# Performance work log

Hardware: AMD Instinct MI355X
Metric: run time of the kernel (lower is better)

The kernel has to match this reference:

```python
import jax, jax.numpy as jnp
import numpy as np
import math

B, S, D, H = 2, 4096, 128, 8

def setup_inputs() -> dict:
    key = jax.random.key(0)
    k1, k2, k3, k4 = jax.random.split(key, 4)
    x = jax.random.normal(k1, (B, S, D), dtype=jnp.float32)
    W_q = jax.random.normal(k2, (H, D, D), dtype=jnp.float32) * 0.02
    W_k = jax.random.normal(k3, (H, D, D), dtype=jnp.float32) * 0.02
    # nn.Linear weight: [out_features, in_features] = [D, D*H]
    W_o = jax.random.normal(k4, (D, D * H), dtype=jnp.float32) * (0.02 / math.sqrt(2 * 12))
    return {"x": x, "W_q": W_q, "W_k": W_k, "W_o": W_o}

def reference(x, W_q, W_k, W_o):
    b, s, d = x.shape
    h = W_q.shape[0]
    # Per-head projections of the same (repeated) input x.
    Q = jnp.einsum('bsd,hde->bhse', x, W_q)          # [B,H,S,D]
    K = jnp.einsum('bsd,hde->bhse', x, W_k)          # [B,H,S,D]
    scores = jnp.einsum('bhse,bhte->bhst', Q, K) / math.sqrt(d)  # [B,H,S,S]
    scores = jnp.clip(scores, -10.0, 10.0)
    causal = jnp.tril(jnp.ones((s, s), dtype=bool))  # [S,S]
    scores = jnp.where(causal[None, None], scores, -jnp.inf)
    attn = jax.nn.softmax(scores, axis=-1)           # dropout p=0 -> identity
    y = jnp.einsum('bhst,btd->bhsd', attn, x)        # V == x per head
    y = jnp.transpose(y, (0, 2, 1, 3)).reshape(b, s, h * d)  # [B,S,H*D]
    out = y @ W_o.T                                  # [B,S,D]
    return out
```

## Files before the change

kernel.cpp:

```cpp
#include <hip/hip_runtime.h>
#include <hip/hip_bf16.h>

typedef unsigned short u16;
typedef unsigned int u32;
typedef __attribute__((ext_vector_type(8))) short bf16x8;
typedef __attribute__((ext_vector_type(4))) float f32x4;
typedef __attribute__((ext_vector_type(16))) float f32x16;
typedef __attribute__((ext_vector_type(2))) unsigned int u32x2;
typedef __attribute__((ext_vector_type(4))) unsigned int u32x4;

#define S_LEN 4096
#define DHEAD 128
#define NHEAD 8
#define NBATCH 2

__device__ __forceinline__ u16 f2b(float f) {
  __hip_bfloat16 h = __float2bfloat16(f);
  return *(u16*)&h;
}

__device__ __forceinline__ f32x4 mfma16(bf16x8 a, bf16x8 b, f32x4 c) {
  return __builtin_amdgcn_mfma_f32_16x16x32_bf16(a, b, c, 0, 0, 0);
}
__device__ __forceinline__ f32x16 mfma32(bf16x8 a, bf16x8 b, f32x16 c) {
  return __builtin_amdgcn_mfma_f32_32x32x16_bf16(a, b, c, 0, 0, 0);
}

__device__ __forceinline__ f32x4 zero4() { f32x4 z = {0.f, 0.f, 0.f, 0.f}; return z; }

__device__ __forceinline__ u32 cvtpk(float lo, float hi) {
  u32 r;
  asm("v_cvt_pk_bf16_f32 %0, %1, %2" : "=v"(r) : "v"(lo), "v"(hi));
  return r;
}
__device__ __forceinline__ u32x2 pswap(u32 a, u32 b) {
  return __builtin_amdgcn_permlane32_swap(a, b, false, false);
}

__device__ __forceinline__ void gll16(const u16* g, u16* l) {
  __builtin_amdgcn_global_load_lds(
      (const __attribute__((address_space(1))) u32*)g,
      (__attribute__((address_space(3))) u32*)l, 16, 0, 0);
}

__global__ void k_conv_x(const float* __restrict__ x, u16* __restrict__ xb,
                         u16* __restrict__ VbF) {
  int idx = blockIdx.x * blockDim.x + threadIdx.x;
  float v = x[idx];
  u16 bv = f2b(v);
  xb[idx] = bv;
  int d = idx & 127;
  int bs = idx >> 7;
  int b = bs >> 12;
  int s = bs & 4095;
  int t64 = s >> 6, kh = (s >> 5) & 1, m2 = (s >> 4) & 1;
  int h5v = (s >> 3) & 1, j = s & 7;
  int db = d >> 5;
  int l = (d & 31) + 32 * h5v;
  int g = kh * 8 + m2 * 4 + db;
  VbF[(((size_t)b * 64 + t64) * 16 + g) * 512 + l * 8 + j] = bv;
}

__global__ void k_conv_w(const float* __restrict__ Wq, const float* __restrict__ Wk,
                         const float* __restrict__ Wo, u16* __restrict__ Wqt,
                         u16* __restrict__ Wkt, u16* __restrict__ WoB) {
  int idx = blockIdx.x * blockDim.x + threadIdx.x;
  int h = idx >> 14;
  int d = (idx >> 7) & 127;
  int e = idx & 127;
  int t = (h << 14) + (e << 7) + d;
  Wqt[t] = f2b(Wq[idx]);
  Wkt[t] = f2b(Wk[idx]);
  WoB[idx] = f2b(Wo[idx]);
}

__global__ __launch_bounds__(256) void k_proj(const u16* __restrict__ xb,
                                              const u16* __restrict__ Wqt,
                                              const u16* __restrict__ Wkt,
                                              u16* __restrict__ Qb, u16* __restrict__ KbF) {
  int wid = threadIdx.x >> 6;
  int lane = threadIdx.x & 63;
  int qt = blockIdx.x * 4 + wid;
  int h = blockIdx.y, z = blockIdx.z;
  int b = z >> 1, w = z & 1;
  int bh = b * NHEAD + h;
  int row16 = lane & 15, kgrp = lane >> 4;
  int sb = qt * 32;
  const u16* xp = xb + ((size_t)b * S_LEN + sb) * DHEAD;
  bf16x8 a[2][4];
#pragma unroll
  for (int r = 0; r < 2; ++r)
#pragma unroll
    for (int kc = 0; kc < 4; ++kc)
      a[r][kc] = *(const bf16x8*)(xp + (r * 16 + row16) * DHEAD + kc * 32 + kgrp * 8);

  const u16* Wt = (w == 0 ? Wqt : Wkt) + (size_t)h * DHEAD * DHEAD;
  f32x4 acc[2][8];
#pragma unroll
  for (int r = 0; r < 2; ++r)
#pragma unroll
    for (int nc = 0; nc < 8; ++nc) acc[r][nc] = zero4();
#pragma unroll
  for (int kc = 0; kc < 4; ++kc)
#pragma unroll
    for (int nc = 0; nc < 8; ++nc) {
      bf16x8 bw = *(const bf16x8*)(Wt + (nc * 16 + row16) * DHEAD + kc * 32 + kgrp * 8);
      acc[0][nc] = mfma16(a[0][kc], bw, acc[0][nc]);
      acc[1][nc] = mfma16(a[1][kc], bw, acc[1][nc]);
    }
  if (w == 0) {
    u16* Out = Qb + ((size_t)bh * S_LEN + sb) * DHEAD;
#pragma unroll
    for (int r = 0; r < 2; ++r)
#pragma unroll
      for (int nc = 0; nc < 8; ++nc)
#pragma unroll
        for (int i = 0; i < 4; ++i)
          Out[(size_t)(r * 16 + kgrp * 4 + i) * DHEAD + nc * 16 + row16] =
              f2b(acc[r][nc][i]);
  } else {
#pragma unroll
    for (int r = 0; r < 2; ++r)
#pragma unroll
      for (int nc = 0; nc < 8; ++nc)
#pragma unroll
        for (int i = 0; i < 4; ++i) {
          int key = sb + r * 16 + kgrp * 4 + i;
          int e = nc * 16 + row16;
          int t64 = key >> 6, kh = (key >> 5) & 1;
          int m = e >> 4;
          int l = (key & 31) + 32 * ((e >> 3) & 1);
          int j = e & 7;
          int f = kh * 8 + m;
          KbF[(((size_t)bh * 64 + t64) * 16 + f) * 512 + l * 8 + j] = f2b(acc[r][nc][i]);
        }
  }
}

__global__ __launch_bounds__(512) void k_attn(const u16* __restrict__ Qb,
                                              const u16* __restrict__ KbF,
                                              const u16* __restrict__ VbF,
                                              u16* __restrict__ Yb) {
  int p = blockIdx.x;
  int xcd = p & 7;
  int j2 = p >> 3;
  int bh = xcd + (j2 >= 16 ? 8 : 0);
  int qpj = j2 & 15;
  int b = bh >> 3, h = bh & 7;

  int tid = threadIdx.x;
  int wid = tid >> 6;
  int lane = tid & 63;
  int qr = wid >> 1;
  int kh = wid & 1;
  int l31 = lane & 31, h5 = lane >> 5;

  __shared__ __align__(16) u16 Klds[2][8192];
  __shared__ __align__(16) u16 Vlds[2][8192];
  __shared__ float rsbuf[2][4][32];

  const u16* Kbase = KbF + (size_t)bh * 64 * 16 * 512;
  const u16* Vbase = VbF + (size_t)b * 64 * 16 * 512;

  auto issue = [&](int k0, int buf) {
    int t64 = k0 >> 6;
    const u16* Ks = Kbase + (size_t)t64 * 16 * 512;
    const u16* Vs = Vbase + (size_t)t64 * 16 * 512;
#pragma unroll
    for (int fi = 0; fi < 2; ++fi) {
      int f = wid * 2 + fi;
      gll16(Ks + f * 512 + lane * 8, &Klds[buf][f * 512]);
    }
#pragma unroll
    for (int gi = 0; gi < 2; ++gi) {
      int g = wid * 2 + gi;
      gll16(Vs + g * 512 + lane * 8, &Vlds[buf][g * 512]);
    }
  };

  const float c2 = 0.12754274816295166f;
  const float clip2 = 14.426950408889634f;

  auto runSeg = [&](int qblk) {
    int qb0 = qblk * 128;
    int qw = qb0 + qr * 32;
    int qrow = qw + l31;
    const u16* Qp = Qb + ((size_t)bh * S_LEN + qw) * DHEAD;

    bf16x8 bq[8];
#pragma unroll
    for (int m = 0; m < 8; ++m)
      bq[m] = *(const bf16x8*)(Qp + (size_t)l31 * DHEAD + m * 16 + h5 * 8);

    f32x16 y0 = {0.f}, y1 = {0.f}, y2 = {0.f}, y3 = {0.f};
#pragma unroll
    for (int i = 0; i < 16; ++i) { y0[i] = 0.f; y1[i] = 0.f; y2[i] = 0.f; y3[i] = 0.f; }
    float rs = 0.f;

    auto tilecomp = [&](int buf, int k0) {
      f32x16 sc;
#pragma unroll
      for (int i = 0; i < 16; ++i) sc[i] = 0.f;
#pragma unroll
      for (int m = 0; m < 8; ++m) {
        bf16x8 kf = *(const bf16x8*)&Klds[buf][((kh * 8 + m) * 512) + lane * 8];
        sc = mfma32(kf, bq[m], sc);
      }
      float pf[16];
      int kb = k0 + kh * 32 + h5 * 4;
#pragma unroll
      for (int reg = 0; reg < 16; ++reg) {
        int key = kb + (reg & 3) + 8 * (reg >> 2);
        float v = sc[reg] * c2;
        v = fminf(fmaxf(v, -clip2), clip2);
        float pc = __builtin_amdgcn_exp2f(v);
        pc = (key > qrow) ? 0.0f : pc;
        rs += pc;
        pf[reg] = pc;
      }
      u32 cv0 = cvtpk(pf[0], pf[1]), cv1 = cvtpk(pf[2], pf[3]);
      u32 cv2 = cvtpk(pf[4], pf[5]), cv3 = cvtpk(pf[6], pf[7]);
      u32 cv4 = cvtpk(pf[8], pf[9]), cv5 = cvtpk(pf[10], pf[11]);
      u32 cv6 = cvtpk(pf[12], pf[13]), cv7 = cvtpk(pf[14], pf[15]);
      u32x2 s0 = pswap(cv0, cv2);
      u32x2 s1 = pswap(cv1, cv3);
      u32x2 s2 = pswap(cv4, cv6);
      u32x2 s3 = pswap(cv5, cv7);
      u32x4 pa0u = {s0.x, s1.x, s0.y, s1.y};
      u32x4 pa1u = {s2.x, s3.x, s2.y, s3.y};
      bf16x8 pa0 = __builtin_bit_cast(bf16x8, pa0u);
      bf16x8 pa1 = __builtin_bit_cast(bf16x8, pa1u);
      {
        bf16x8 vf = *(const bf16x8*)&Vlds[buf][((kh * 8 + 0) * 512) + lane * 8];
        y0 = mfma32(pa0, vf, y0);
        vf = *(const bf16x8*)&Vlds[buf][((kh * 8 + 4) * 512) + lane * 8];
        y0 = mfma32(pa1, vf, y0);
        vf = *(const bf16x8*)&Vlds[buf][((kh * 8 + 1) * 512) + lane * 8];
        y1 = mfma32(pa0, vf, y1);
        vf = *(const bf16x8*)&Vlds[buf][((kh * 8 + 5) * 512) + lane * 8];
        y1 = mfma32(pa1, vf, y1);
        vf = *(const bf16x8*)&Vlds[buf][((kh * 8 + 2) * 512) + lane * 8];
        y2 = mfma32(pa0, vf, y2);
        vf = *(const bf16x8*)&Vlds[buf][((kh * 8 + 6) * 512) + lane * 8];
        y2 = mfma32(pa1, vf, y2);
        vf = *(const bf16x8*)&Vlds[buf][((kh * 8 + 3) * 512) + lane * 8];
        y3 = mfma32(pa0, vf, y3);
        vf = *(const bf16x8*)&Vlds[buf][((kh * 8 + 7) * 512) + lane * 8];
        y3 = mfma32(pa1, vf, y3);
      }
    };

    int NT = 2 * qblk + 2;
    issue(0, 0);
    __syncthreads();
    for (int t = 0; t < NT; ++t) {
      int k0 = t * 64;
      int cur = t & 1;
      if (t + 1 < NT) issue(k0 + 64, cur ^ 1);
      tilecomp(cur, k0);
      __syncthreads();
    }

    rs += __shfl_xor(rs, 32, 64);

    float* scr = (qr < 2) ? ((float*)&Klds[0][0] + qr * 4096)
                          : ((float*)&Vlds[0][0] + (qr - 2) * 4096);
    if (kh == 1) {
#pragma unroll
      for (int db = 0; db < 4; ++db) {
        const f32x16& yv = (db == 0) ? y0 : (db == 1) ? y1 : (db == 2) ? y2 : y3;
#pragma unroll
        for (int r4 = 0; r4 < 4; ++r4) {
          f32x4 ch = {yv[r4 * 4 + 0], yv[r4 * 4 + 1], yv[r4 * 4 + 2], yv[r4 * 4 + 3]};
          *(f32x4*)&scr[((db * 4 + r4) * 64 + lane) * 4] = ch;
        }
      }
      if (lane < 32) rsbuf[1][qr][lane] = rs;
    }
    __syncthreads();
    if (kh == 0) {
      rs += rsbuf[1][qr][l31];
      float inv = 1.0f / rs;
      if (lane < 32) rsbuf[0][qr][lane] = inv;
#pragma unroll
      for (int db = 0; db < 4; ++db) {
        f32x16& yv = (db == 0) ? y0 : (db == 1) ? y1 : (db == 2) ? y2 : y3;
#pragma unroll
        for (int r4 = 0; r4 < 4; ++r4) {
          f32x4 ch = *(const f32x4*)&scr[((db * 4 + r4) * 64 + lane) * 4];
#pragma unroll
          for (int k = 0; k < 4; ++k) yv[r4 * 4 + k] += ch[k];
        }
      }
      u16* Yp = Yb + ((size_t)b * S_LEN + qw) * (NHEAD * DHEAD) + h * DHEAD;
#pragma unroll
      for (int db = 0; db < 4; ++db) {
        const f32x16& yv = (db == 0) ? y0 : (db == 1) ? y1 : (db == 2) ? y2 : y3;
#pragma unroll
        for (int reg = 0; reg < 16; ++reg) {
          int qp2 = (reg & 3) + 8 * (reg >> 2) + 4 * h5;
          float rv = rsbuf[0][qr][qp2];
          Yp[(size_t)qp2 * (NHEAD * DHEAD) + db * 32 + l31] = f2b(yv[reg] * rv);
        }
      }
    }
    __syncthreads();
  };

  runSeg(31 - qpj);
  runSeg(qpj);
}

__global__ __launch_bounds__(256) void k_oproj(const u16* __restrict__ Yb,
                                               const u16* __restrict__ WoB,
                                               float* __restrict__ out) {
  int wid = threadIdx.x >> 6;
  int lane = threadIdx.x & 63;
  int mb = (blockIdx.x * 4 + wid) * 32 + blockIdx.y * 16;
  int nb = blockIdx.z * 64;
  int row16 = lane & 15, kgrp = lane >> 4;
  f32x4 acc[4];
#pragma unroll
  for (int nc = 0; nc < 4; ++nc) acc[nc] = zero4();
#pragma unroll 4
  for (int kc = 0; kc < 32; ++kc) {
    bf16x8 a0 = *(const bf16x8*)(Yb + (size_t)(mb + row16) * 1024 + kc * 32 + kgrp * 8);
#pragma unroll
    for (int nc = 0; nc < 4; ++nc) {
      bf16x8 bw =
          *(const bf16x8*)(WoB + (size_t)(nb + nc * 16 + row16) * 1024 + kc * 32 + kgrp * 8);
      acc[nc] = mfma16(a0, bw, acc[nc]);
    }
  }
#pragma unroll
  for (int nc = 0; nc < 4; ++nc)
#pragma unroll
    for (int i = 0; i < 4; ++i)
      out[(size_t)(mb + kgrp * 4 + i) * DHEAD + nb + nc * 16 + row16] = acc[nc][i];
}

extern "C" void kernel_launch(void* const* d_in, const int* in_sizes, int n_in,
                              void* d_out, int out_size, void* d_ws, size_t ws_size,
                              hipStream_t stream) {
  const float* x = (const float*)d_in[0];
  const float* Wq = (const float*)d_in[1];
  const float* Wk = (const float*)d_in[2];
  const float* Wo = (const float*)d_in[3];
  float* out = (float*)d_out;

  char* ws = (char*)d_ws;
  size_t off = 0;
  auto alloc = [&](size_t bytes) -> void* {
    void* p = ws + off;
    off += (bytes + 255) & ~(size_t)255;
    return p;
  };
  const size_t nx = (size_t)NBATCH * S_LEN * DHEAD;
  const size_t nqk = (size_t)NBATCH * NHEAD * S_LEN * DHEAD;
  u16* xb = (u16*)alloc(nx * 2);
  u16* VbF = (u16*)alloc(nx * 2);
  u16* Wqt = (u16*)alloc((size_t)NHEAD * DHEAD * DHEAD * 2);
  u16* Wkt = (u16*)alloc((size_t)NHEAD * DHEAD * DHEAD * 2);
  u16* WoB = (u16*)alloc((size_t)DHEAD * NHEAD * DHEAD * 2);
  u16* Qb = (u16*)alloc(nqk * 2);
  u16* KbF = (u16*)alloc(nqk * 2);
  u16* Yb = (u16*)alloc(nqk * 2);
  (void)ws_size;

  k_conv_x<<<dim3(nx / 256), dim3(256), 0, stream>>>(x, xb, VbF);
  k_conv_w<<<dim3(131072 / 256), dim3(256), 0, stream>>>(Wq, Wk, Wo, Wqt, Wkt, WoB);
  k_proj<<<dim3(S_LEN / 32 / 4, NHEAD, 2 * NBATCH), dim3(256), 0, stream>>>(xb, Wqt, Wkt, Qb, KbF);
  k_attn<<<dim3(256), dim3(512), 0, stream>>>(Qb, KbF, VbF, Yb);
  k_oproj<<<dim3((NBATCH * S_LEN) / 32 / 4, 2, 2), dim3(256), 0, stream>>>(Yb, WoB, out);
}
```

Before: 164.9 us.

## Load V fragments directly to registers, prefetch next tile, skip masking on full tiles

V tiles are no longer staged through LDS. Each wave loads its V fragments from global memory straight into registers, double-buffered one tile ahead, while K stays in LDS. The loop is unrolled by two so buffer indices are static, mask computation is skipped for tiles fully below the diagonal, clamping uses fmed3, and setprio brackets the MFMA bursts. The cross-wave reduction now uses a separate float scratch buffer in two phases. This frees LDS and cuts LDS traffic, at the cost of more registers and uncoalesced-per-wave global V reads.

Result: faster. 158.4 us (-4.0%).

```diff
diff --git a/kernel.cpp b/kernel.cpp
--- a/kernel.cpp
+++ b/kernel.cpp
@@ -156,26 +156,24 @@
   int l31 = lane & 31, h5 = lane >> 5;
 
   __shared__ __align__(16) u16 Klds[2][8192];
-  __shared__ __align__(16) u16 Vlds[2][8192];
+  __shared__ __align__(16) float Scr[8192];
   __shared__ float rsbuf[2][4][32];
 
   const u16* Kbase = KbF + (size_t)bh * 64 * 16 * 512;
   const u16* Vbase = VbF + (size_t)b * 64 * 16 * 512;
 
   auto issue = [&](int k0, int buf) {
-    int t64 = k0 >> 6;
-    const u16* Ks = Kbase + (size_t)t64 * 16 * 512;
-    const u16* Vs = Vbase + (size_t)t64 * 16 * 512;
+    const u16* Ks = Kbase + (size_t)(k0 >> 6) * 16 * 512;
 #pragma unroll
     for (int fi = 0; fi < 2; ++fi) {
       int f = wid * 2 + fi;
       gll16(Ks + f * 512 + lane * 8, &Klds[buf][f * 512]);
     }
-#pragma unroll
-    for (int gi = 0; gi < 2; ++gi) {
-      int g = wid * 2 + gi;
-      gll16(Vs + g * 512 + lane * 8, &Vlds[buf][g * 512]);
-    }
+  };
+  auto vload = [&](bf16x8 (&dst)[8], int k0) {
+    const u16* Vs = Vbase + ((size_t)(k0 >> 6) * 16 + kh * 8) * 512 + lane * 8;
+#pragma unroll
+    for (int g = 0; g < 8; ++g) dst[g] = *(const bf16x8*)(Vs + g * 512);
   };
 
   const float c2 = 0.12754274816295166f;
@@ -192,31 +190,47 @@
     for (int m = 0; m < 8; ++m)
       bq[m] = *(const bf16x8*)(Qp + (size_t)l31 * DHEAD + m * 16 + h5 * 8);
 
-    f32x16 y0 = {0.f}, y1 = {0.f}, y2 = {0.f}, y3 = {0.f};
+    f32x16 y0, y1, y2, y3;
 #pragma unroll
     for (int i = 0; i < 16; ++i) { y0[i] = 0.f; y1[i] = 0.f; y2[i] = 0.f; y3[i] = 0.f; }
     float rs = 0.f;
 
-    auto tilecomp = [&](int buf, int k0) {
+    bf16x8 vA[8], vB[8];
+
+    auto tilecomp = [&](int buf, int k0, bf16x8 (&vc)[8], bf16x8 (&vn)[8], int kn0) {
       f32x16 sc;
 #pragma unroll
       for (int i = 0; i < 16; ++i) sc[i] = 0.f;
+      __builtin_amdgcn_s_setprio(1);
 #pragma unroll
       for (int m = 0; m < 8; ++m) {
         bf16x8 kf = *(const bf16x8*)&Klds[buf][((kh * 8 + m) * 512) + lane * 8];
         sc = mfma32(kf, bq[m], sc);
       }
+      __builtin_amdgcn_s_setprio(0);
+      vload(vn, kn0);
+
       float pf[16];
       int kb = k0 + kh * 32 + h5 * 4;
-#pragma unroll
-      for (int reg = 0; reg < 16; ++reg) {
-        int key = kb + (reg & 3) + 8 * (reg >> 2);
-        float v = sc[reg] * c2;
-        v = fminf(fmaxf(v, -clip2), clip2);
-        float pc = __builtin_amdgcn_exp2f(v);
-        pc = (key > qrow) ? 0.0f : pc;
-        rs += pc;
-        pf[reg] = pc;
+      bool nomask = (k0 + kh * 32 + 31) <= qw;
+      if (nomask) {
+#pragma unroll
+        for (int reg = 0; reg < 16; ++reg) {
+          float v = __builtin_amdgcn_fmed3f(sc[reg] * c2, -clip2, clip2);
+          float pc = __builtin_amdgcn_exp2f(v);
+          rs += pc;
+          pf[reg] = pc;
+        }
+      } else {
+#pragma unroll
+        for (int reg = 0; reg < 16; ++reg) {
+          int key = kb + (reg & 3) + 8 * (reg >> 2);
+          float v = __builtin_amdgcn_fmed3f(sc[reg] * c2, -clip2, clip2);
+          float pc = __builtin_amdgcn_exp2f(v);
+          pc = (key > qrow) ? 0.0f : pc;
+          rs += pc;
+          pf[reg] = pc;
+        }
       }
       u32 cv0 = cvtpk(pf[0], pf[1]), cv1 = cvtpk(pf[2], pf[3]);
       u32 cv2 = cvtpk(pf[4], pf[5]), cv3 = cvtpk(pf[6], pf[7]);
@@ -230,81 +244,80 @@
       u32x4 pa1u = {s2.x, s3.x, s2.y, s3.y};
       bf16x8 pa0 = __builtin_bit_cast(bf16x8, pa0u);
       bf16x8 pa1 = __builtin_bit_cast(bf16x8, pa1u);
-      {
-        bf16x8 vf = *(const bf16x8*)&Vlds[buf][((kh * 8 + 0) * 512) + lane * 8];
-        y0 = mfma32(pa0, vf, y0);
-        vf = *(const bf16x8*)&Vlds[buf][((kh * 8 + 4) * 512) + lane * 8];
-        y0 = mfma32(pa1, vf, y0);
-        vf = *(const bf16x8*)&Vlds[buf][((kh * 8 + 1) * 512) + lane * 8];
-        y1 = mfma32(pa0, vf, y1);
-        vf = *(const bf16x8*)&Vlds[buf][((kh * 8 + 5) * 512) + lane * 8];
-        y1 = mfma32(pa1, vf, y1);
-        vf = *(const bf16x8*)&Vlds[buf][((kh * 8 + 2) * 512) + lane * 8];
-        y2 = mfma32(pa0, vf, y2);
-        vf = *(const bf16x8*)&Vlds[buf][((kh * 8 + 6) * 512) + lane * 8];
-        y2 = mfma32(pa1, vf, y2);
-        vf = *(const bf16x8*)&Vlds[buf][((kh * 8 + 3) * 512) + lane * 8];
-        y3 = mfma32(pa0, vf, y3);
-        vf = *(const bf16x8*)&Vlds[buf][((kh * 8 + 7) * 512) + lane * 8];
-        y3 = mfma32(pa1, vf, y3);
-      }
+      __builtin_amdgcn_s_setprio(1);
+      y0 = mfma32(pa0, vc[0], y0);
+      y0 = mfma32(pa1, vc[4], y0);
+      y1 = mfma32(pa0, vc[1], y1);
+      y1 = mfma32(pa1, vc[5], y1);
+      y2 = mfma32(pa0, vc[2], y2);
+      y2 = mfma32(pa1, vc[6], y2);
+      y3 = mfma32(pa0, vc[3], y3);
+      y3 = mfma32(pa1, vc[7], y3);
+      __builtin_amdgcn_s_setprio(0);
     };
 
     int NT = 2 * qblk + 2;
     issue(0, 0);
+    vload(vA, 0);
     __syncthreads();
-    for (int t = 0; t < NT; ++t) {
+    for (int t = 0; t < NT; t += 2) {
       int k0 = t * 64;
-      int cur = t & 1;
-      if (t + 1 < NT) issue(k0 + 64, cur ^ 1);
-      tilecomp(cur, k0);
+      issue(k0 + 64, 1);
+      tilecomp(0, k0, vA, vB, k0 + 64);
       __syncthreads();
+      int k1 = k0 + 64;
+      bool more = (t + 2 < NT);
+      if (more) issue(k1 + 64, 0);
+      tilecomp(1, k1, vB, vA, more ? k1 + 64 : k1);
+      __syncthreads();
     }
 
     rs += __shfl_xor(rs, 32, 64);
 
-    float* scr = (qr < 2) ? ((float*)&Klds[0][0] + qr * 4096)
-                          : ((float*)&Vlds[0][0] + (qr - 2) * 4096);
-    if (kh == 1) {
-#pragma unroll
-      for (int db = 0; db < 4; ++db) {
-        const f32x16& yv = (db == 0) ? y0 : (db == 1) ? y1 : (db == 2) ? y2 : y3;
-#pragma unroll
-        for (int r4 = 0; r4 < 4; ++r4) {
-          f32x4 ch = {yv[r4 * 4 + 0], yv[r4 * 4 + 1], yv[r4 * 4 + 2], yv[r4 * 4 + 3]};
-          *(f32x4*)&scr[((db * 4 + r4) * 64 + lane) * 4] = ch;
-        }
+#pragma unroll
+    for (int pr = 0; pr < 2; ++pr) {
+      float* scr = Scr + (qr >> 1) * 4096;
+      if ((qr & 1) == pr && kh == 1) {
+#pragma unroll
+        for (int db = 0; db < 4; ++db) {
+          const f32x16& yv = (db == 0) ? y0 : (db == 1) ? y1 : (db == 2) ? y2 : y3;
+#pragma unroll
+          for (int r4 = 0; r4 < 4; ++r4) {
+            f32x4 ch = {yv[r4 * 4 + 0], yv[r4 * 4 + 1], yv[r4 * 4 + 2], yv[r4 * 4 + 3]};
+            *(f32x4*)&scr[((db * 4 + r4) * 64 + lane) * 4] = ch;
+          }
+        }
+        if (lane < 32) rsbuf[1][qr][lane] = rs;
       }
-      if (lane < 32) rsbuf[1][qr][lane] = rs;
-    }
-    __syncthreads();
-    if (kh == 0) {
-      rs += rsbuf[1][qr][l31];
-      float inv = 1.0f / rs;
-      if (lane < 32) rsbuf[0][qr][lane] = inv;
-#pragma unroll
-      for (int db = 0; db < 4; ++db) {
-        f32x16& yv = (db == 0) ? y0 : (db == 1) ? y1 : (db == 2) ? y2 : y3;
-#pragma unroll
-        for (int r4 = 0; r4 < 4; ++r4) {
-          f32x4 ch = *(const f32x4*)&scr[((db * 4 + r4) * 64 + lane) * 4];
-#pragma unroll
-          for (int k = 0; k < 4; ++k) yv[r4 * 4 + k] += ch[k];
+      __syncthreads();
+      if ((qr & 1) == pr && kh == 0) {
+        float rs2 = rs + rsbuf[1][qr][l31];
+        float inv = 1.0f / rs2;
+        if (lane < 32) rsbuf[0][qr][lane] = inv;
+#pragma unroll
+        for (int db = 0; db < 4; ++db) {
+          f32x16& yv = (db == 0) ? y0 : (db == 1) ? y1 : (db == 2) ? y2 : y3;
+#pragma unroll
+          for (int r4 = 0; r4 < 4; ++r4) {
+            f32x4 ch = *(const f32x4*)&scr[((db * 4 + r4) * 64 + lane) * 4];
+#pragma unroll
+            for (int k = 0; k < 4; ++k) yv[r4 * 4 + k] += ch[k];
+          }
+        }
+        u16* Yp = Yb + ((size_t)b * S_LEN + qw) * (NHEAD * DHEAD) + h * DHEAD;
+#pragma unroll
+        for (int db = 0; db < 4; ++db) {
+          const f32x16& yv = (db == 0) ? y0 : (db == 1) ? y1 : (db == 2) ? y2 : y3;
+#pragma unroll
+          for (int reg = 0; reg < 16; ++reg) {
+            int qp2 = (reg & 3) + 8 * (reg >> 2) + 4 * h5;
+            float rv = rsbuf[0][qr][qp2];
+            Yp[(size_t)qp2 * (NHEAD * DHEAD) + db * 32 + l31] = f2b(yv[reg] * rv);
+          }
         }
       }
-      u16* Yp = Yb + ((size_t)b * S_LEN + qw) * (NHEAD * DHEAD) + h * DHEAD;
-#pragma unroll
-      for (int db = 0; db < 4; ++db) {
-        const f32x16& yv = (db == 0) ? y0 : (db == 1) ? y1 : (db == 2) ? y2 : y3;
-#pragma unroll
-        for (int reg = 0; reg < 16; ++reg) {
-          int qp2 = (reg & 3) + 8 * (reg >> 2) + 4 * h5;
-          float rv = rsbuf[0][qr][qp2];
-          Yp[(size_t)qp2 * (NHEAD * DHEAD) + db * 32 + l31] = f2b(yv[reg] * rv);
-        }
-      }
-    }
-    __syncthreads();
+      __syncthreads();
+    }
   };
 
   runSeg(31 - qpj);
```
